# Kernel optimization log

Measured on AMD Instinct MI355X. Metric: run time of the kernel, lower is better.

Reference implementation:

```python
import jax, jax.numpy as jnp
import numpy as np

SUPPORT_FACTOR = 2.5
EPSILON = 1e-5


def setup_inputs() -> dict:
    key = jax.random.key(0)
    k1, _ = jax.random.split(key)
    # 64x64 regular particle grid on [0,1]^2 -> N = 4096 nodes
    n_side = 64
    g = jnp.linspace(0.0, 1.0, n_side, dtype=jnp.float32)
    gx, gy = jnp.meshgrid(g, g, indexing='ij')
    nodes = jnp.stack([gx.ravel(), gy.ravel()], axis=-1)  # [4096, 2]
    # B = 4096 query (collocation) points inside the same domain
    x = jax.random.uniform(k1, (4096, 2), dtype=jnp.float32)
    return {"x": x, "nodes": nodes}


def _cubic_spline(q):
    # piecewise cubic spline kernel; zero outside q > 1
    w_inner = 2.0 / 3.0 - 4.0 * q ** 2 + 4.0 * q ** 3          # q <= 0.5
    w_outer = 4.0 / 3.0 - 4.0 * q + 4.0 * q ** 2 - (4.0 / 3.0) * q ** 3  # 0.5 < q <= 1
    return jnp.where(q <= 0.5, w_inner, jnp.where(q <= 1.0, w_outer, 0.0))


def _dilation(nodes):
    # support_factor * mean nearest-neighbor spacing (replaces init-time cKDTree)
    d2 = jnp.sum((nodes[:, None, :] - nodes[None, :, :]) ** 2, axis=-1)  # [N, N]
    d2 = d2 + jnp.where(jnp.eye(nodes.shape[0], dtype=bool), jnp.inf, 0.0)
    h_avg = jnp.mean(jnp.sqrt(jnp.min(d2, axis=1)))
    return SUPPORT_FACTOR * h_avg


def reference(x, nodes):
    dilation = _dilation(nodes)
    diff = x[:, None, :] - nodes[None, :, :]          # [B, N, 2]
    dx = diff[..., 0]
    dy = diff[..., 1]
    dist = jnp.sqrt(dx ** 2 + dy ** 2 + 1e-10)        # [B, N]
    q = dist / dilation
    w = _cubic_spline(q) * (q <= 1.0)                 # support-radius mask
    ones = jnp.ones_like(dx)
    P = jnp.stack([ones, dx, dy], axis=-1)            # [B, N, 3]
    M = jnp.einsum('bni,bnj,bn->bij', P, P, w)        # [B, 3, 3] moment matrices
    M_reg = M + jnp.eye(3, dtype=x.dtype) * EPSILON
    M_inv = jnp.linalg.inv(M_reg)                     # batched 3x3 inverse
    P_w = P * w[..., None]
    b_vec = jnp.einsum('bij,bnj->bni', M_inv, P_w)    # [B, N, 3]
    phi = b_vec[..., 0]
    phi_x = -b_vec[..., 1]
    phi_y = -b_vec[..., 2]
    return (phi, phi_x, phi_y)
```

## Files before the change

### kernel.cpp

```cpp
#include <hip/hip_runtime.h>

#define N_NODES 4096
#define B_PTS   4096
#define SUPPORT_FACTOR 2.5f
#define EPSILON 1e-5f

__global__ __launch_bounds__(256) void nearest_kernel(
        const float* __restrict__ nodes, float* __restrict__ mind) {
    const int i = blockIdx.x;
    const float xi = nodes[2 * i];
    const float yi = nodes[2 * i + 1];

    const float4* nodes4 = (const float4*)nodes;
    float mind2 = 3.4e38f;
    for (int k = threadIdx.x; k < N_NODES / 2; k += 256) {
        float4 v = nodes4[k];
        float dx0 = xi - v.x, dy0 = yi - v.y;
        float dx1 = xi - v.z, dy1 = yi - v.w;
        float d20 = dx0 * dx0 + dy0 * dy0;
        float d21 = dx1 * dx1 + dy1 * dy1;
        if (2 * k != i)     mind2 = fminf(mind2, d20);
        if (2 * k + 1 != i) mind2 = fminf(mind2, d21);
    }
    #pragma unroll
    for (int off = 32; off > 0; off >>= 1)
        mind2 = fminf(mind2, __shfl_down(mind2, off, 64));

    __shared__ float sw[4];
    const int wave = threadIdx.x >> 6;
    if ((threadIdx.x & 63) == 0) sw[wave] = mind2;
    __syncthreads();
    if (threadIdx.x == 0) {
        float m = fminf(fminf(sw[0], sw[1]), fminf(sw[2], sw[3]));
        mind[i] = sqrtf(m);
    }
}

__global__ __launch_bounds__(256) void dil_kernel(float* __restrict__ mind) {
    __shared__ float sw[4];
    const int tid = threadIdx.x;
    const float4* m4 = (const float4*)mind;
    float s = 0.f;
    #pragma unroll
    for (int k = 0; k < 4; ++k) {
        float4 v = m4[k * 256 + tid];
        s += (v.x + v.y) + (v.z + v.w);
    }
    #pragma unroll
    for (int off = 32; off > 0; off >>= 1)
        s += __shfl_down(s, off, 64);
    if ((tid & 63) == 0) sw[tid >> 6] = s;
    __syncthreads();
    if (tid == 0) {
        float dil = (sw[0] + sw[1] + sw[2] + sw[3]) *
                    (SUPPORT_FACTOR / (float)N_NODES);
        mind[0] = 1.0f / dil;
        mind[1] = dil * dil * 1.0002f + 1e-9f;
    }
}

__device__ __forceinline__ float cubic_w(float q) {
    if (q <= 0.5f) return 2.0f / 3.0f + q * q * (4.0f * q - 4.0f);
    if (q <= 1.0f) return 4.0f / 3.0f + q * (-4.0f + q * (4.0f - (4.0f / 3.0f) * q));
    return 0.0f;
}

__global__ __launch_bounds__(256) void rkpm_sparse(
        const float* __restrict__ x, const float* __restrict__ nodes,
        const float* __restrict__ dilp, float* __restrict__ out) {
    __shared__ float sred[4][6];
    __shared__ float sbc[9];

    const int b = blockIdx.x;
    const int tid = threadIdx.x;
    const int wave = tid >> 6;
    const int lane = tid & 63;

    const size_t BN = (size_t)B_PTS * N_NODES;
    float* __restrict__ row0 = out + (size_t)b * N_NODES;
    float* __restrict__ row1 = row0 + BN;
    float* __restrict__ row2 = row1 + BN;

    {
        float4 z4; z4.x = 0.f; z4.y = 0.f; z4.z = 0.f; z4.w = 0.f;
        float4* p0 = (float4*)row0;
        float4* p1 = (float4*)row1;
        float4* p2 = (float4*)row2;
        #pragma unroll
        for (int k = 0; k < 4; ++k) {
            p0[k * 256 + tid] = z4;
            p1[k * 256 + tid] = z4;
            p2[k * 256 + tid] = z4;
        }
    }

    const float inv_dil = dilp[0];
    const float r2m     = dilp[1];
    const float2 xq = ((const float2*)x)[b];
    const float xb = xq.x, yb = xq.y;

    const float4* nodes4 = (const float4*)nodes;
    float m00 = 0.f, m01 = 0.f, m02 = 0.f, m11 = 0.f, m12 = 0.f, m22 = 0.f;
    #pragma unroll
    for (int kk = 0; kk < 4; ++kk) {
        float4 va = nodes4[kk * 512 + 2 * tid];
        float4 vb = nodes4[kk * 512 + 2 * tid + 1];
        float dx0 = xb - va.x, dy0 = yb - va.y;
        float dx1 = xb - va.z, dy1 = yb - va.w;
        float dx2 = xb - vb.x, dy2 = yb - vb.y;
        float dx3 = xb - vb.z, dy3 = yb - vb.w;
        float d0 = dx0 * dx0 + dy0 * dy0;
        float d1 = dx1 * dx1 + dy1 * dy1;
        float d2 = dx2 * dx2 + dy2 * dy2;
        float d3 = dx3 * dx3 + dy3 * dy3;
        float dmin = fminf(fminf(d0, d1), fminf(d2, d3));
        if (dmin <= r2m) {
            float w0 = cubic_w(sqrtf(d0 + 1e-10f) * inv_dil);
            float w1 = cubic_w(sqrtf(d1 + 1e-10f) * inv_dil);
            float w2 = cubic_w(sqrtf(d2 + 1e-10f) * inv_dil);
            float w3 = cubic_w(sqrtf(d3 + 1e-10f) * inv_dil);
            m00 += (w0 + w1) + (w2 + w3);
            m01 += (w0 * dx0 + w1 * dx1) + (w2 * dx2 + w3 * dx3);
            m02 += (w0 * dy0 + w1 * dy1) + (w2 * dy2 + w3 * dy3);
            m11 += (w0 * dx0 * dx0 + w1 * dx1 * dx1) + (w2 * dx2 * dx2 + w3 * dx3 * dx3);
            m12 += (w0 * dx0 * dy0 + w1 * dx1 * dy1) + (w2 * dx2 * dy2 + w3 * dx3 * dy3);
            m22 += (w0 * dy0 * dy0 + w1 * dy1 * dy1) + (w2 * dy2 * dy2 + w3 * dy3 * dy3);
        }
    }
    #pragma unroll
    for (int off = 32; off > 0; off >>= 1) {
        m00 += __shfl_down(m00, off, 64);
        m01 += __shfl_down(m01, off, 64);
        m02 += __shfl_down(m02, off, 64);
        m11 += __shfl_down(m11, off, 64);
        m12 += __shfl_down(m12, off, 64);
        m22 += __shfl_down(m22, off, 64);
    }
    if (lane == 0) {
        sred[wave][0] = m00; sred[wave][1] = m01; sred[wave][2] = m02;
        sred[wave][3] = m11; sred[wave][4] = m12; sred[wave][5] = m22;
    }
    __syncthreads();

    if (tid == 0) {
        float a  = sred[0][0] + sred[1][0] + sred[2][0] + sred[3][0] + EPSILON;
        float bb = sred[0][1] + sred[1][1] + sred[2][1] + sred[3][1];
        float c  = sred[0][2] + sred[1][2] + sred[2][2] + sred[3][2];
        float d  = sred[0][3] + sred[1][3] + sred[2][3] + sred[3][3] + EPSILON;
        float e  = sred[0][4] + sred[1][4] + sred[2][4] + sred[3][4];
        float f  = sred[0][5] + sred[1][5] + sred[2][5] + sred[3][5] + EPSILON;
        float c00 = d * f - e * e;
        float c01 = c * e - bb * f;
        float c02 = bb * e - c * d;
        float det = a * c00 + bb * c01 + c * c02;
        float idet = 1.0f / det;
        float i00 = c00 * idet;
        float i01 = c01 * idet;
        float i02 = c02 * idet;
        float i11 = (a * f - c * c) * idet;
        float i12 = (bb * c - a * e) * idet;
        float i22 = (a * d - bb * bb) * idet;
        sbc[0] = i00;  sbc[1] = i01;  sbc[2] = i02;
        sbc[3] = -i01; sbc[4] = -i11; sbc[5] = -i12;
        sbc[6] = -i02; sbc[7] = -i12; sbc[8] = -i22;
    }
    __syncthreads();

    const float i00 = sbc[0], i01 = sbc[1], i02  = sbc[2];
    const float n01 = sbc[3], n11 = sbc[4], n12  = sbc[5];
    const float n02 = sbc[6], n12b = sbc[7], n22 = sbc[8];

    #define SCATTER(DX, DY, DD, J)                                          \
        {                                                                   \
            float w_ = cubic_w(sqrtf((DD) + 1e-10f) * inv_dil);             \
            if (w_ != 0.0f) {                                               \
                row0[J] = w_ * (i00 + i01 * (DX) + i02  * (DY));            \
                row1[J] = w_ * (n01 + n11 * (DX) + n12  * (DY));            \
                row2[J] = w_ * (n02 + n12b * (DX) + n22 * (DY));            \
            }                                                               \
        }

    #pragma unroll
    for (int kk = 0; kk < 4; ++kk) {
        float4 va = nodes4[kk * 512 + 2 * tid];
        float4 vb = nodes4[kk * 512 + 2 * tid + 1];
        float dx0 = xb - va.x, dy0 = yb - va.y;
        float dx1 = xb - va.z, dy1 = yb - va.w;
        float dx2 = xb - vb.x, dy2 = yb - vb.y;
        float dx3 = xb - vb.z, dy3 = yb - vb.w;
        float d0 = dx0 * dx0 + dy0 * dy0;
        float d1 = dx1 * dx1 + dy1 * dy1;
        float d2 = dx2 * dx2 + dy2 * dy2;
        float d3 = dx3 * dx3 + dy3 * dy3;
        float dmin = fminf(fminf(d0, d1), fminf(d2, d3));
        if (dmin <= r2m) {
            const int j = kk * 1024 + 4 * tid;
            SCATTER(dx0, dy0, d0, j);
            SCATTER(dx1, dy1, d1, j + 1);
            SCATTER(dx2, dy2, d2, j + 2);
            SCATTER(dx3, dy3, d3, j + 3);
        }
    }
    #undef SCATTER
}

extern "C" void kernel_launch(void* const* d_in, const int* in_sizes, int n_in,
                              void* d_out, int out_size, void* d_ws, size_t ws_size,
                              hipStream_t stream) {
    const float* x     = (const float*)d_in[0];
    const float* nodes = (const float*)d_in[1];
    float* out  = (float*)d_out;
    float* mind = (float*)d_ws;

    nearest_kernel<<<N_NODES, 256, 0, stream>>>(nodes, mind);
    dil_kernel<<<1, 256, 0, stream>>>(mind);
    rkpm_sparse<<<B_PTS, 256, 0, stream>>>(x, nodes, mind, out);
}
```

Baseline: 211.0 us.

## Fuse dilation reduction into main kernel and write outputs once with nontemporal vector stores

```diff
diff --git a/kernel.cpp b/kernel.cpp
--- a/kernel.cpp
+++ b/kernel.cpp
@@ -4,6 +4,8 @@
 #define B_PTS   4096
 #define SUPPORT_FACTOR 2.5f
 #define EPSILON 1e-5f
+
+typedef float fx4 __attribute__((ext_vector_type(4)));
 
 __global__ __launch_bounds__(256) void nearest_kernel(
         const float* __restrict__ nodes, float* __restrict__ mind) {
@@ -11,10 +13,10 @@
     const float xi = nodes[2 * i];
     const float yi = nodes[2 * i + 1];
 
-    const float4* nodes4 = (const float4*)nodes;
+    const fx4* nodes4 = (const fx4*)nodes;
     float mind2 = 3.4e38f;
     for (int k = threadIdx.x; k < N_NODES / 2; k += 256) {
-        float4 v = nodes4[k];
+        fx4 v = nodes4[k];
         float dx0 = xi - v.x, dy0 = yi - v.y;
         float dx1 = xi - v.z, dy1 = yi - v.w;
         float d20 = dx0 * dx0 + dy0 * dy0;
@@ -36,75 +38,54 @@
     }
 }
 
-__global__ __launch_bounds__(256) void dil_kernel(float* __restrict__ mind) {
-    __shared__ float sw[4];
-    const int tid = threadIdx.x;
-    const float4* m4 = (const float4*)mind;
-    float s = 0.f;
-    #pragma unroll
-    for (int k = 0; k < 4; ++k) {
-        float4 v = m4[k * 256 + tid];
-        s += (v.x + v.y) + (v.z + v.w);
-    }
-    #pragma unroll
-    for (int off = 32; off > 0; off >>= 1)
-        s += __shfl_down(s, off, 64);
-    if ((tid & 63) == 0) sw[tid >> 6] = s;
-    __syncthreads();
-    if (tid == 0) {
-        float dil = (sw[0] + sw[1] + sw[2] + sw[3]) *
-                    (SUPPORT_FACTOR / (float)N_NODES);
-        mind[0] = 1.0f / dil;
-        mind[1] = dil * dil * 1.0002f + 1e-9f;
-    }
-}
-
 __device__ __forceinline__ float cubic_w(float q) {
     if (q <= 0.5f) return 2.0f / 3.0f + q * q * (4.0f * q - 4.0f);
     if (q <= 1.0f) return 4.0f / 3.0f + q * (-4.0f + q * (4.0f - (4.0f / 3.0f) * q));
     return 0.0f;
 }
 
-__global__ __launch_bounds__(256) void rkpm_sparse(
+__global__ __launch_bounds__(256) void rkpm_kernel(
         const float* __restrict__ x, const float* __restrict__ nodes,
-        const float* __restrict__ dilp, float* __restrict__ out) {
+        const float* __restrict__ mind, float* __restrict__ out) {
     __shared__ float sred[4][6];
-    __shared__ float sbc[9];
+    __shared__ float sbc[10];
 
     const int b = blockIdx.x;
     const int tid = threadIdx.x;
     const int wave = tid >> 6;
     const int lane = tid & 63;
 
-    const size_t BN = (size_t)B_PTS * N_NODES;
-    float* __restrict__ row0 = out + (size_t)b * N_NODES;
-    float* __restrict__ row1 = row0 + BN;
-    float* __restrict__ row2 = row1 + BN;
-
-    {
-        float4 z4; z4.x = 0.f; z4.y = 0.f; z4.z = 0.f; z4.w = 0.f;
-        float4* p0 = (float4*)row0;
-        float4* p1 = (float4*)row1;
-        float4* p2 = (float4*)row2;
-        #pragma unroll
-        for (int k = 0; k < 4; ++k) {
-            p0[k * 256 + tid] = z4;
-            p1[k * 256 + tid] = z4;
-            p2[k * 256 + tid] = z4;
-        }
-    }
-
-    const float inv_dil = dilp[0];
-    const float r2m     = dilp[1];
+    const fx4* m4 = (const fx4*)mind;
+    float s = 0.f;
+    #pragma unroll
+    for (int k = 0; k < 4; ++k) {
+        fx4 v = m4[k * 256 + tid];
+        s += (v.x + v.y) + (v.z + v.w);
+    }
+    #pragma unroll
+    for (int off = 32; off > 0; off >>= 1)
+        s += __shfl_down(s, off, 64);
+    if (lane == 0) sred[wave][0] = s;
+    __syncthreads();
+    if (tid == 0) {
+        float dil = (sred[0][0] + sred[1][0] + sred[2][0] + sred[3][0]) *
+                    (SUPPORT_FACTOR / (float)N_NODES);
+        sbc[0] = 1.0f / dil;
+        sbc[1] = dil * dil * 1.0002f + 1e-9f;
+    }
+    __syncthreads();
+    const float inv_dil = sbc[0];
+    const float r2m     = sbc[1];
+
     const float2 xq = ((const float2*)x)[b];
     const float xb = xq.x, yb = xq.y;
 
-    const float4* nodes4 = (const float4*)nodes;
+    const fx4* nodes4 = (const fx4*)nodes;
     float m00 = 0.f, m01 = 0.f, m02 = 0.f, m11 = 0.f, m12 = 0.f, m22 = 0.f;
     #pragma unroll
     for (int kk = 0; kk < 4; ++kk) {
-        float4 va = nodes4[kk * 512 + 2 * tid];
-        float4 vb = nodes4[kk * 512 + 2 * tid + 1];
+        fx4 va = nodes4[kk * 512 + 2 * tid];
+        fx4 vb = nodes4[kk * 512 + 2 * tid + 1];
         float dx0 = xb - va.x, dy0 = yb - va.y;
         float dx1 = xb - va.z, dy1 = yb - va.w;
         float dx2 = xb - vb.x, dy2 = yb - vb.y;
@@ -160,30 +141,25 @@
         float i11 = (a * f - c * c) * idet;
         float i12 = (bb * c - a * e) * idet;
         float i22 = (a * d - bb * bb) * idet;
-        sbc[0] = i00;  sbc[1] = i01;  sbc[2] = i02;
-        sbc[3] = -i01; sbc[4] = -i11; sbc[5] = -i12;
-        sbc[6] = -i02; sbc[7] = -i12; sbc[8] = -i22;
-    }
-    __syncthreads();
-
-    const float i00 = sbc[0], i01 = sbc[1], i02  = sbc[2];
-    const float n01 = sbc[3], n11 = sbc[4], n12  = sbc[5];
-    const float n02 = sbc[6], n12b = sbc[7], n22 = sbc[8];
-
-    #define SCATTER(DX, DY, DD, J)                                          \
-        {                                                                   \
-            float w_ = cubic_w(sqrtf((DD) + 1e-10f) * inv_dil);             \
-            if (w_ != 0.0f) {                                               \
-                row0[J] = w_ * (i00 + i01 * (DX) + i02  * (DY));            \
-                row1[J] = w_ * (n01 + n11 * (DX) + n12  * (DY));            \
-                row2[J] = w_ * (n02 + n12b * (DX) + n22 * (DY));            \
-            }                                                               \
-        }
+        sbc[1] = i00;  sbc[2] = i01;  sbc[3] = i02;
+        sbc[4] = -i01; sbc[5] = -i11; sbc[6] = -i12;
+        sbc[7] = -i02; sbc[8] = -i12; sbc[9] = -i22;
+    }
+    __syncthreads();
+
+    const float i00 = sbc[1], i01 = sbc[2], i02  = sbc[3];
+    const float n01 = sbc[4], n11 = sbc[5], n12  = sbc[6];
+    const float n02 = sbc[7], n12b = sbc[8], n22 = sbc[9];
+
+    const size_t BN = (size_t)B_PTS * N_NODES;
+    fx4* __restrict__ out_phi = (fx4*)(out + (size_t)b * N_NODES);
+    fx4* __restrict__ out_px  = (fx4*)(out + BN + (size_t)b * N_NODES);
+    fx4* __restrict__ out_py  = (fx4*)(out + 2 * BN + (size_t)b * N_NODES);
 
     #pragma unroll
     for (int kk = 0; kk < 4; ++kk) {
-        float4 va = nodes4[kk * 512 + 2 * tid];
-        float4 vb = nodes4[kk * 512 + 2 * tid + 1];
+        fx4 va = nodes4[kk * 512 + 2 * tid];
+        fx4 vb = nodes4[kk * 512 + 2 * tid + 1];
         float dx0 = xb - va.x, dy0 = yb - va.y;
         float dx1 = xb - va.z, dy1 = yb - va.w;
         float dx2 = xb - vb.x, dy2 = yb - vb.y;
@@ -193,15 +169,33 @@
         float d2 = dx2 * dx2 + dy2 * dy2;
         float d3 = dx3 * dx3 + dy3 * dy3;
         float dmin = fminf(fminf(d0, d1), fminf(d2, d3));
+
+        fx4 ph = {0.f, 0.f, 0.f, 0.f};
+        fx4 px = {0.f, 0.f, 0.f, 0.f};
+        fx4 py = {0.f, 0.f, 0.f, 0.f};
         if (dmin <= r2m) {
-            const int j = kk * 1024 + 4 * tid;
-            SCATTER(dx0, dy0, d0, j);
-            SCATTER(dx1, dy1, d1, j + 1);
-            SCATTER(dx2, dy2, d2, j + 2);
-            SCATTER(dx3, dy3, d3, j + 3);
+            float w0 = cubic_w(sqrtf(d0 + 1e-10f) * inv_dil);
+            float w1 = cubic_w(sqrtf(d1 + 1e-10f) * inv_dil);
+            float w2 = cubic_w(sqrtf(d2 + 1e-10f) * inv_dil);
+            float w3 = cubic_w(sqrtf(d3 + 1e-10f) * inv_dil);
+            ph.x = w0 * (i00 + i01 * dx0 + i02 * dy0);
+            ph.y = w1 * (i00 + i01 * dx1 + i02 * dy1);
+            ph.z = w2 * (i00 + i01 * dx2 + i02 * dy2);
+            ph.w = w3 * (i00 + i01 * dx3 + i02 * dy3);
+            px.x = w0 * (n01 + n11 * dx0 + n12 * dy0);
+            px.y = w1 * (n01 + n11 * dx1 + n12 * dy1);
+            px.z = w2 * (n01 + n11 * dx2 + n12 * dy2);
+            px.w = w3 * (n01 + n11 * dx3 + n12 * dy3);
+            py.x = w0 * (n02 + n12b * dx0 + n22 * dy0);
+            py.y = w1 * (n02 + n12b * dx1 + n22 * dy1);
+            py.z = w2 * (n02 + n12b * dx2 + n22 * dy2);
+            py.w = w3 * (n02 + n12b * dx3 + n22 * dy3);
         }
-    }
-    #undef SCATTER
+        const int idx = kk * 256 + tid;
+        __builtin_nontemporal_store(ph, out_phi + idx);
+        __builtin_nontemporal_store(px, out_px + idx);
+        __builtin_nontemporal_store(py, out_py + idx);
+    }
 }
 
 extern "C" void kernel_launch(void* const* d_in, const int* in_sizes, int n_in,
@@ -213,6 +207,5 @@
     float* mind = (float*)d_ws;
 
     nearest_kernel<<<N_NODES, 256, 0, stream>>>(nodes, mind);
-    dil_kernel<<<1, 256, 0, stream>>>(mind);
-    rkpm_sparse<<<B_PTS, 256, 0, stream>>>(x, nodes, mind, out);
-}
+    rkpm_kernel<<<B_PTS, 256, 0, stream>>>(x, nodes, mind, out);
+}
```

Measured after the change: 214.2 us. No clear change (+1.5%).
